# Optimization experiments

Measured on AMD Instinct MI355X. Metric: run time of the kernel, lower is better.

Reference implementation:

```python
import jax, jax.numpy as jnp
import numpy as np

CE_W, BOUND_W, DICE_W, SMOOTH = 1.0, 0.1, 1.0, 1e-6


def setup_inputs() -> dict:
    key = jax.random.key(0)
    k1, k2 = jax.random.split(key)
    B, C, H, W = 8, 1, 256, 256
    logits = jax.random.normal(k1, (B, C, H, W), dtype=jnp.float32)
    target = jax.random.uniform(k2, (B, C, H, W), dtype=jnp.float32)
    return {"logits": logits, "target": target}


def _edt(fg):
    # fg: [B, H, W] bool foreground mask. Returns exact Euclidean distance
    # transform of the background (0 at foreground), matching
    # scipy.ndimage.distance_transform_edt(1 - fg).
    B, H, W = fg.shape
    INF = jnp.float32(H + W)  # larger than any in-image 1D distance

    # --- pass 1: vertical distance to nearest foreground in each column ---
    fg_t = jnp.transpose(fg, (1, 0, 2))  # [H, B, W], scan over rows

    def step(carry, fg_row):
        d = jnp.where(fg_row, 0.0, carry + 1.0)
        return d, d

    init = jnp.full((B, W), INF, dtype=jnp.float32)
    _, g_fwd = jax.lax.scan(step, init, fg_t)                 # top-down
    _, g_bwd = jax.lax.scan(step, init, fg_t, reverse=True)   # bottom-up
    g = jnp.minimum(g_fwd, g_bwd)          # [H, B, W]
    g = jnp.transpose(g, (1, 0, 2))        # [B, H, W]

    # --- pass 2: exact squared EDT per row: min_k (j-k)^2 + g[i,k]^2 ---
    j = jnp.arange(W, dtype=jnp.float32)
    offs2 = (j[:, None] - j[None, :]) ** 2                    # [W, W]
    # [B, H, Wj, Wk] intermediate -> min over k
    dt2 = jnp.min(g[:, :, None, :] ** 2 + offs2[None, None, :, :], axis=-1)
    dt = jnp.sqrt(dt2)

    # empty masks get an all-zero distance map (scipy branch in the original)
    nonempty = jnp.any(fg, axis=(1, 2))
    return jnp.where(nonempty[:, None, None], dt, 0.0)


def reference(logits, target):
    target = jnp.clip(target.astype(jnp.float32), 0.0, 1.0)

    # BCEWithLogitsLoss (mean): stable log(1 + e^x) - x*t
    ce = jnp.mean(jnp.logaddexp(0.0, logits) - logits * target)

    probs = jnp.clip(jax.nn.sigmoid(logits), SMOOTH, 1.0 - SMOOTH)

    # Dice over flattened tensors
    p, t = probs.reshape(-1), target.reshape(-1)
    inter = jnp.sum(p * t)
    dice = 1.0 - (2.0 * inter + SMOOTH) / (jnp.sum(p) + jnp.sum(t) + SMOOTH)

    # Boundary: mean(probs * EDT(target > 0.5)) -- EDT is non-differentiable data
    fg = target[:, 0] > 0.5                      # [B, H, W]
    dt = jax.lax.stop_gradient(_edt(fg))[:, None]  # [B, 1, H, W]
    boundary = jnp.mean(probs * dt)

    total = CE_W * ce + DICE_W * dice + BOUND_W * boundary
    return total, ce, dice, boundary
```

## Files before the change

### kernel.cpp

```cpp
#include <hip/hip_runtime.h>

#define BB 8
#define HH 256
#define WW 256
#define NTOT (BB * HH * WW)
#define RPB 8
#define NBLK (BB * HH / RPB)

__global__ __launch_bounds__(256) void mega_kernel(
    const float* __restrict__ logits, const float* __restrict__ target,
    float* __restrict__ partials ) {
  __shared__ float s_g2[RPB][3 * WW];
  __shared__ float s_red[4 * 5];
  __shared__ int s_im[4 * 2];

  const int g = blockIdx.x;
  const int b = g >> 5;
  const int i0 = (g & 31) * RPB;
  const int j = threadIdx.x;
  const int lane = j & 63, wave = j >> 6;

  const float* col = target + b * (HH * WW) + j;
  unsigned m[8];
#pragma unroll
  for (int w = 0; w < 8; ++w) {
    unsigned mw = 0;
#pragma unroll
    for (int r = 0; r < 32; ++r)
      if (col[(w * 32 + r) * WW] > 0.5f) mw |= (1u << r);
    m[w] = mw;
  }
  const unsigned many = m[0] | m[1] | m[2] | m[3] | m[4] | m[5] | m[6] | m[7];

  int rmax = 0;
#pragma unroll
  for (int r = 0; r < RPB; ++r) {
    const int i = i0 + r;
    const int wi = i >> 5, rr = i & 31;
    int dUp = 1 << 30, dDn = 1 << 30;
    const unsigned cur = m[wi] >> rr;
    if (cur) {
      dUp = __builtin_ctz(cur);
    } else {
      int off = 32 - rr;
      for (int w2 = wi + 1; w2 < 8; ++w2, off += 32)
        if (m[w2]) { dUp = off + __builtin_ctz(m[w2]); break; }
    }
    const unsigned curd = m[wi] << (31 - rr);
    if (curd) {
      dDn = __builtin_clz(curd);
    } else {
      int off = rr + 1;
      for (int w2 = wi - 1; w2 >= 0; --w2, off += 32)
        if (m[w2]) { dDn = off + __builtin_clz(m[w2]); break; }
    }
    const int d = min(dUp, dDn);
    s_g2[r][WW + j] = (d < 256) ? (float)(d * d) : 1.0e9f;
    s_g2[r][j] = 1.0e9f;
    s_g2[r][2 * WW + j] = 1.0e9f;
    rmax = max(rmax, min(d, 255));
  }

  const int wave_any = __any(many != 0u);
#pragma unroll
  for (int off = 32; off > 0; off >>= 1)
    rmax = max(rmax, __shfl_down(rmax, off, 64));
  if (lane == 0) { s_im[wave * 2] = wave_any; s_im[wave * 2 + 1] = rmax; }
  __syncthreads();
  const int nonempty = s_im[0] | s_im[2] | s_im[4] | s_im[6];
  const int R = max(max(s_im[1], s_im[3]), max(s_im[5], s_im[7]));

  float v0 = 0.f, v1 = 0.f, v2 = 0.f, v3 = 0.f, v4 = 0.f;
#pragma unroll
  for (int r = 0; r < RPB; ++r) {
    float mn = 1.0e30f;
    const float* gp = &s_g2[r][WW + j];
    for (int dlt = -R; dlt <= R; ++dlt)
      mn = fminf(mn, (float)(dlt * dlt) + gp[dlt]);
    const float dt = nonempty ? sqrtf(mn) : 0.0f;

    const int idx = (b * HH + i0 + r) * WW + j;
    const float x = logits[idx];
    float t = target[idx];
    t = fminf(fmaxf(t, 0.0f), 1.0f);
    const float e = __expf(-fabsf(x));
    const float inv = 1.0f / (1.0f + e);
    const float ce = fmaxf(x, 0.0f) + __logf(1.0f + e) - x * t;
    float p = (x >= 0.0f) ? inv : e * inv;
    p = fminf(fmaxf(p, 1e-6f), 1.0f - 1e-6f);
    v0 += ce; v1 += p; v2 += t; v3 += p * t; v4 += p * dt;
  }

  float v[5] = {v0, v1, v2, v3, v4};
#pragma unroll
  for (int q = 0; q < 5; ++q) {
    float s = v[q];
#pragma unroll
    for (int off = 32; off > 0; off >>= 1) s += __shfl_down(s, off, 64);
    if (lane == 0) s_red[wave * 5 + q] = s;
  }
  __syncthreads();
  if (j == 0) {
#pragma unroll
    for (int q = 0; q < 5; ++q)
      partials[q * NBLK + g] =
          s_red[q] + s_red[5 + q] + s_red[10 + q] + s_red[15 + q];
  }
}

__global__ __launch_bounds__(256) void finalize(
    const float* __restrict__ partials, float* __restrict__ out) {
  __shared__ double s_red[4 * 5];
  const int j = threadIdx.x;
  const int lane = j & 63, wave = j >> 6;
  double acc[5];
#pragma unroll
  for (int q = 0; q < 5; ++q) acc[q] = (double)partials[q * NBLK + j];
#pragma unroll
  for (int q = 0; q < 5; ++q) {
    double s = acc[q];
#pragma unroll
    for (int off = 32; off > 0; off >>= 1) s += __shfl_down(s, off, 64);
    if (lane == 0) s_red[wave * 5 + q] = s;
  }
  __syncthreads();
  if (j == 0) {
    double sum[5];
#pragma unroll
    for (int q = 0; q < 5; ++q)
      sum[q] = s_red[q] + s_red[5 + q] + s_red[10 + q] + s_red[15 + q];
    const double n = (double)NTOT;
    const double ce = sum[0] / n;
    const double dice = 1.0 - (2.0 * sum[3] + 1e-6) / (sum[1] + sum[2] + 1e-6);
    const double boundary = sum[4] / n;
    out[0] = (float)(ce + dice + 0.1 * boundary);
    out[1] = (float)ce;
    out[2] = (float)dice;
    out[3] = (float)boundary;
  }
}

extern "C" void kernel_launch(void* const* d_in, const int* in_sizes, int n_in,
                              void* d_out, int out_size, void* d_ws,
                              size_t ws_size, hipStream_t stream) {
  const float* logits = (const float*)d_in[0];
  const float* target = (const float*)d_in[1];
  float* out = (float*)d_out;

  float* partials = (float*)d_ws;

  mega_kernel<<<NBLK, 256, 0, stream>>>(logits, target, partials);
  finalize<<<1, 256, 0, stream>>>(partials, out);
}
```

Before: 77.93 us.

## Replace full-column mask scan with early-exit local search for vertical distances

Before, every block loaded its image's entire 256-row column of target to build bitmasks for the vertical distance pass. Now each block loads only its own 8 rows, then scans upward and downward in chunks of 8 rows. A chunked scan stops as soon as every lane in the wave has found a foreground pixel. This removes most of the redundant target reads, which were repeated by all 32 blocks of each image. The cost is data-dependent loops with wave votes, so sparse masks fall back to long scans.

New measurement: 78.22 us. Within noise of the previous version (+0.4%).

```diff
diff --git a/kernel.cpp b/kernel.cpp
--- a/kernel.cpp
+++ b/kernel.cpp
@@ -20,48 +20,60 @@
   const int j = threadIdx.x;
   const int lane = j & 63, wave = j >> 6;
 
-  const float* col = target + b * (HH * WW) + j;
-  unsigned m[8];
+  const float* img = target + b * (HH * WW);
+
+  unsigned m8 = 0;
 #pragma unroll
-  for (int w = 0; w < 8; ++w) {
-    unsigned mw = 0;
+  for (int r = 0; r < RPB; ++r)
+    if (img[(i0 + r) * WW + j] > 0.5f) m8 |= (1u << r);
+
+  const int INFD = 1 << 24;
+  int kUp = INFD;
+  bool fUp = (m8 & 1u) != 0u;
+  bool sawUp = false;
+  for (int k0 = 0; k0 < i0 && !__all(fUp); k0 += 8) {
+    bool fgv[8];
 #pragma unroll
-    for (int r = 0; r < 32; ++r)
-      if (col[(w * 32 + r) * WW] > 0.5f) mw |= (1u << r);
-    m[w] = mw;
+    for (int kk = 0; kk < 8; ++kk) {
+      const int k = k0 + kk;
+      fgv[kk] = (k < i0) && (img[(i0 - 1 - k) * WW + j] > 0.5f);
+    }
+#pragma unroll
+    for (int kk = 0; kk < 8; ++kk)
+      if (!fUp && fgv[kk]) { kUp = k0 + kk; fUp = true; sawUp = true; }
   }
-  const unsigned many = m[0] | m[1] | m[2] | m[3] | m[4] | m[5] | m[6] | m[7];
+
+  const int limDn = HH - i0 - RPB;
+  int kDn = INFD;
+  bool fDn = (m8 >> (RPB - 1)) & 1u;
+  bool sawDn = false;
+  for (int k0 = 0; k0 < limDn && !__all(fDn); k0 += 8) {
+    bool fgv[8];
+#pragma unroll
+    for (int kk = 0; kk < 8; ++kk) {
+      const int k = k0 + kk;
+      fgv[kk] = (k < limDn) && (img[(i0 + RPB + k) * WW + j] > 0.5f);
+    }
+#pragma unroll
+    for (int kk = 0; kk < 8; ++kk)
+      if (!fDn && fgv[kk]) { kDn = k0 + kk; fDn = true; sawDn = true; }
+  }
 
   int rmax = 0;
 #pragma unroll
   for (int r = 0; r < RPB; ++r) {
-    const int i = i0 + r;
-    const int wi = i >> 5, rr = i & 31;
-    int dUp = 1 << 30, dDn = 1 << 30;
-    const unsigned cur = m[wi] >> rr;
-    if (cur) {
-      dUp = __builtin_ctz(cur);
-    } else {
-      int off = 32 - rr;
-      for (int w2 = wi + 1; w2 < 8; ++w2, off += 32)
-        if (m[w2]) { dUp = off + __builtin_ctz(m[w2]); break; }
-    }
-    const unsigned curd = m[wi] << (31 - rr);
-    if (curd) {
-      dDn = __builtin_clz(curd);
-    } else {
-      int off = rr + 1;
-      for (int w2 = wi - 1; w2 >= 0; --w2, off += 32)
-        if (m[w2]) { dDn = off + __builtin_clz(m[w2]); break; }
-    }
-    const int d = min(dUp, dDn);
+    const unsigned hi = m8 >> r;
+    const int dA = hi ? __builtin_ctz(hi) : (RPB - r + kDn);
+    const unsigned lo = m8 & ((1u << (r + 1)) - 1u);
+    const int dB = lo ? (r - (31 - __builtin_clz(lo))) : (r + 1 + kUp);
+    const int d = min(dA, dB);
     s_g2[r][WW + j] = (d < 256) ? (float)(d * d) : 1.0e9f;
     s_g2[r][j] = 1.0e9f;
     s_g2[r][2 * WW + j] = 1.0e9f;
     rmax = max(rmax, min(d, 255));
   }
 
-  const int wave_any = __any(many != 0u);
+  const int wave_any = __any((m8 != 0u) | sawUp | sawDn);
 #pragma unroll
   for (int off = 32; off > 0; off >>= 1)
     rmax = max(rmax, __shfl_down(rmax, off, 64));
@@ -81,7 +93,7 @@
 
     const int idx = (b * HH + i0 + r) * WW + j;
     const float x = logits[idx];
-    float t = target[idx];
+    float t = img[(i0 + r) * WW + j];
     t = fminf(fmaxf(t, 0.0f), 1.0f);
     const float e = __expf(-fabsf(x));
     const float inv = 1.0f / (1.0f + e);
```
